# Kernel optimization log

Hardware: AMD Instinct MI355X
Metric: run time of the kernel (lower is better)

## Reference

```python
import jax, jax.numpy as jnp
import numpy as np

NEG_INF = -1e10
LEAKY_ALPHA = 0.2


def setup_inputs() -> dict:
    key = jax.random.key(0)
    k1, k2, k3, k4, k5 = jax.random.split(key, 5)
    N, F, H, D = 4096, 512, 8, 64
    X = jax.random.normal(k1, (N, F), dtype=jnp.float32)
    # dense 0/1 adjacency (float, as used by the mask formula)
    A = jax.random.randint(k2, (N, N), 0, 2).astype(jnp.float32)
    W = jax.random.normal(k3, (H, F, D), dtype=jnp.float32) * (1.0 / np.sqrt(F))
    b = jnp.zeros((H, D), dtype=jnp.float32)
    a_self = jax.random.normal(k4, (H, D), dtype=jnp.float32) * (1.0 / np.sqrt(D))
    a_neigh = jax.random.normal(k5, (H, D), dtype=jnp.float32) * (1.0 / np.sqrt(D))
    return {"X": X, "A": A, "W": W, "b": b, "a_self": a_self, "a_neigh": a_neigh}


def reference(X, A, W, b, a_self, a_neigh):
    # Multi-head dense GAT, heads vectorized. Dropout is identity (eval mode).
    # feats: [H, N, D]
    feats = jnp.einsum('nf,hfd->hnd', X, W)
    e_self = jnp.einsum('hnd,hd->hn', feats, a_self)    # [H, N]
    e_neigh = jnp.einsum('hnd,hd->hn', feats, a_neigh)  # [H, N]
    # outer-sum additive scores: [H, N, N]
    dense = e_self[:, :, None] + e_neigh[:, None, :]
    dense = jnp.where(dense >= 0, dense, LEAKY_ALPHA * dense)  # LeakyReLU(0.2)
    mask = NEG_INF * (1.0 - A)                                  # [N, N]
    dense = dense + mask[None, :, :]
    attn = jax.nn.softmax(dense, axis=-1)                       # [H, N, N]
    out = jnp.einsum('hnm,hmd->hnd', attn, feats) + b[:, None, :]
    # concat heads -> [N, H*D], then relu activation
    H, N, D = out.shape
    out = jnp.transpose(out, (1, 0, 2)).reshape(N, H * D)
    return jax.nn.relu(out)
```

## Files before the change

kernel.cpp:

```cpp
#include <hip/hip_runtime.h>
#include <hip/hip_fp16.h>
#include <stdint.h>


#define NODES 4096
#define FEAT  512
#define HEADS 8
#define DH    64
#define NT    (NODES / 64)

using half2v = __attribute__((ext_vector_type(2))) _Float16;
using half8  = __attribute__((ext_vector_type(8))) _Float16;
using f32x4  = __attribute__((ext_vector_type(4))) float;

__device__ __forceinline__ void gll16(const void* g, void* l) {
    __builtin_amdgcn_global_load_lds(
        (const __attribute__((address_space(1))) uint32_t*)g,
        (__attribute__((address_space(3))) uint32_t*)l, 16, 0, 0);
}

__device__ __forceinline__ uint32_t fenc(float f) {
    uint32_t u = __float_as_uint(f);
    return (u >> 31) ? ~u : (u | 0x80000000u);
}
__device__ __forceinline__ float fdec(uint32_t e) {
    uint32_t u = (e >> 31) ? (e & 0x7FFFFFFFu) : ~e;
    return __uint_as_float(u);
}

#define PACK_BLOCKS 16384
#define CAST_BLOCKS (NODES * FEAT / 4 / 256)
#define WT_BLOCKS   (HEADS * 8)

__global__ __launch_bounds__(256) void prep_kernel(
    const float* __restrict__ A, const float* __restrict__ X, const float* __restrict__ W,
    uint64_t* __restrict__ AbitsT, _Float16* __restrict__ Xh, _Float16* __restrict__ WT,
    uint32_t* __restrict__ enmax_u) {
    __shared__ float t[64][65];
    const int bx = blockIdx.x;
    if (bx < PACK_BLOCKS) {
        const int w    = threadIdx.x >> 6;
        const int lane = threadIdx.x & 63;
        const int v    = bx * 4 + w;
        const int wc   = v >> 10;
        const int rowb = (v & 1023) * 4;
        const float* ar = A + (size_t)wc * 64 + lane;
#pragma unroll
        for (int tt = 0; tt < 4; ++tt) {
            uint64_t m = __ballot(ar[(size_t)(rowb + tt) * NODES] != 0.0f);
            if (lane == 0) AbitsT[(size_t)wc * NODES + rowb + tt] = m;
        }
        return;
    }
    if (bx < PACK_BLOCKS + CAST_BLOCKS) {
        if (bx == PACK_BLOCKS && threadIdx.x < 16) enmax_u[threadIdx.x] = 0;
        int i = ((bx - PACK_BLOCKS) * 256 + threadIdx.x) * 4;
        f32x4 x = *(const f32x4*)(X + i);
        *(half2v*)(Xh + i)     = half2v{(_Float16)x[0], (_Float16)x[1]};
        *(half2v*)(Xh + i + 2) = half2v{(_Float16)x[2], (_Float16)x[3]};
        return;
    }
    const int b2 = bx - PACK_BLOCKS - CAST_BLOCKS;
    const int h  = b2 >> 3;
    const int ft = b2 & 7;
    const int r  = threadIdx.x >> 6;
    const int c  = threadIdx.x & 63;
#pragma unroll
    for (int r0 = 0; r0 < 64; r0 += 4)
        t[r0 + r][c] = W[((size_t)h * FEAT + ft * 64 + r0 + r) * DH + c];
    __syncthreads();
#pragma unroll
    for (int r0 = 0; r0 < 64; r0 += 4)
        WT[((size_t)h * DH + r0 + r) * FEAT + ft * 64 + c] = (_Float16)t[c][r0 + r];
}

__global__ __launch_bounds__(256) void feats_kernel(
    const _Float16* __restrict__ Xh, const _Float16* __restrict__ WT,
    const float* __restrict__ a_self, const float* __restrict__ a_neigh,
    _Float16* __restrict__ Vt, float* __restrict__ e_self,
    _Float16* __restrict__ u_tab, _Float16* __restrict__ v_tab,
    uint32_t* __restrict__ enmax_u) {
    const int h    = blockIdx.y;
    const int bx   = blockIdx.x;
    const int tid  = threadIdx.x;
    const int w    = tid >> 6;
    const int lane = tid & 63;
    const int l15  = lane & 15;
    const int g    = lane >> 4;
    const int n0   = bx * 64 + w * 16;

    f32x4 acc[4] = {};
    const _Float16* xb = Xh + (n0 + l15) * FEAT + g * 8;
    const _Float16* wb = WT + (h * DH + l15) * FEAT + g * 8;

#pragma unroll
    for (int kk = 0; kk < FEAT / 32; ++kk) {
        half8 b = *(const half8*)(xb + kk * 32);
#pragma unroll
        for (int mi = 0; mi < 4; ++mi) {
            half8 a = *(const half8*)(wb + mi * 16 * FEAT + kk * 32);
            acc[mi] = __builtin_amdgcn_mfma_f32_16x16x32_f16(a, b, acc[mi], 0, 0, 0);
        }
    }

    const int cc = w * 2 + (l15 >> 3);
    const int e  = l15 & 7;
    float ps = 0.f, pn = 0.f;
#pragma unroll
    for (int mi = 0; mi < 4; ++mi) {
#pragma unroll
        for (int r = 0; r < 4; ++r) {
            int d = mi * 16 + g * 4 + r;
            float v = acc[mi][r];
            Vt[((size_t)h * NT + bx) * 4096 + cc * 512 + d * 8 + e] = (_Float16)v;
            ps += v * a_self[h * DH + d];
            pn += v * a_neigh[h * DH + d];
        }
    }
    ps += __shfl_xor(ps, 16); ps += __shfl_xor(ps, 32);
    pn += __shfl_xor(pn, 16); pn += __shfl_xor(pn, 32);
    if (g == 0) {
        int n = n0 + l15;
        e_self[h * NODES + n] = ps;
        u_tab[h * NODES + n]  = (_Float16)__expf(pn);
        v_tab[h * NODES + n]  = (_Float16)__expf(0.2f * pn);
    }
    float mx = pn;
    mx = fmaxf(mx, __shfl_xor(mx, 1));
    mx = fmaxf(mx, __shfl_xor(mx, 2));
    mx = fmaxf(mx, __shfl_xor(mx, 4));
    mx = fmaxf(mx, __shfl_xor(mx, 8));
    if (lane == 0) atomicMax(enmax_u + h, fenc(mx));
}

__global__ __launch_bounds__(256, 4) void attn_kernel(
    const uint64_t* __restrict__ AbitsT, const _Float16* __restrict__ Vt,
    const float* __restrict__ e_self, const _Float16* __restrict__ u_tab,
    const _Float16* __restrict__ v_tab, const uint32_t* __restrict__ enmax_u,
    const float* __restrict__ bias, float* __restrict__ out) {
    __shared__ __align__(16) _Float16 Vlds[2][2][4096];
    float* redf = (float*)&Vlds[0][0][0];

    const int tid  = threadIdx.x;
    const int w    = tid >> 6;
    const int lane = tid & 63;
    const int l15  = lane & 15;
    const int g    = lane >> 4;
    const int g8   = g * 8;
    const int rh   = w & 1;
    const int jq   = w >> 1;
    const int h    = blockIdx.x & 7;
    const int i0   = (blockIdx.x >> 3) * 32;

    const float em = fdec(enmax_u[h]);
    const float es = e_self[h * NODES + i0 + rh * 16 + l15];
    const float t0 = es + em;
    const float M  = fmaxf(t0, 0.2f * t0);
    const _Float16 c1 = (_Float16)__expf(es - M);
    const _Float16 c2 = (_Float16)__expf(0.2f * es - M);
    const half2v c1h = half2v{c1, c1};
    const half2v c2h = half2v{c2, c2};

    const _Float16* ub  = u_tab + h * NODES + jq * 2048 + g8;
    const _Float16* vb  = v_tab + h * NODES + jq * 2048 + g8;
    const uint64_t* ab  = AbitsT + (size_t)(jq * 32) * NODES + i0 + rh * 16 + l15;
    const _Float16* vtb = Vt + ((size_t)h * NT + jq * 32) * 4096;

#define STAGE(s_, buf_) do {                                        \
        const _Float16* vs_ = vtb + (size_t)(s_) * 4096;            \
        _Float16* vd_ = &Vlds[jq][buf_][0];                         \
        _Pragma("unroll")                                           \
        for (int p_ = 0; p_ < 4; ++p_) {                            \
            const int c_ = rh * 256 + p_ * 64 + lane;               \
            gll16(vs_ + c_ * 8, vd_ + c_ * 8);                      \
        }                                                           \
    } while (0)

    f32x4 acc[4] = {};
    f32x4 asum = {};
    half8 ones;
#pragma unroll
    for (int e = 0; e < 8; ++e) ones[e] = (_Float16)1.0f;

    STAGE(0, 0);
    uint64_t wb_c = ab[0];
    half8 uf_c[2], vf_c[2];
#pragma unroll
    for (int kk = 0; kk < 2; ++kk) {
        uf_c[kk] = *(const half8*)(ub + kk * 32);
        vf_c[kk] = *(const half8*)(vb + kk * 32);
    }
    __syncthreads();

    for (int s = 0; s < 32; ++s) {
        const int buf = s & 1;
        STAGE(s + 1, buf ^ 1);
        uint64_t wb_n = ab[(size_t)(s + 1) * NODES];
        half8 uf_n[2], vf_n[2];
#pragma unroll
        for (int kk = 0; kk < 2; ++kk) {
            uf_n[kk] = *(const half8*)(ub + (s + 1) * 64 + kk * 32);
            vf_n[kk] = *(const half8*)(vb + (s + 1) * 64 + kk * 32);
        }

        const _Float16* vl = &Vlds[jq][buf][0];
#pragma unroll
        for (int kk = 0; kk < 2; ++kk) {
            const uint32_t b0 = ((uint32_t)(wb_c >> (kk * 32)) >> g8) & 0xFFu;
            half8 paf;
#pragma unroll
            for (int q = 0; q < 4; ++q) {
                half2v u2 = half2v{uf_c[kk][2 * q], uf_c[kk][2 * q + 1]};
                half2v v2 = half2v{vf_c[kk][2 * q], vf_c[kk][2 * q + 1]};
                half2v p2 = __builtin_elementwise_max(u2 * c1h, v2 * c2h);
                uint32_t mlo = (uint32_t)(-(int32_t)((b0 >> (2 * q)) & 1u));
                uint32_t mhi = (uint32_t)(-(int32_t)((b0 >> (2 * q + 1)) & 1u));
                uint32_t m = (mhi & 0xFFFF0000u) | (mlo & 0xFFFFu);
                p2 = __builtin_bit_cast(half2v, __builtin_bit_cast(uint32_t, p2) & m);
                paf[2 * q] = p2[0]; paf[2 * q + 1] = p2[1];
            }
            __builtin_amdgcn_s_setprio(1);
#pragma unroll
            for (int ni = 0; ni < 4; ++ni) {
                const half8 vfr = *(const half8*)(vl + (kk * 4 + g) * 512 + (ni * 16 + l15) * 8);
                acc[ni] = __builtin_amdgcn_mfma_f32_16x16x32_f16(paf, vfr, acc[ni], 0, 0, 0);
            }
            asum = __builtin_amdgcn_mfma_f32_16x16x32_f16(paf, ones, asum, 0, 0, 0);
            __builtin_amdgcn_s_setprio(0);
        }
        wb_c = wb_n;
#pragma unroll
        for (int kk = 0; kk < 2; ++kk) { uf_c[kk] = uf_n[kk]; vf_c[kk] = vf_n[kk]; }
        __syncthreads();
    }

    if (jq == 1) {
#pragma unroll
        for (int ni = 0; ni < 4; ++ni)
#pragma unroll
            for (int r = 0; r < 4; ++r)
                redf[(rh * 16 + g * 4 + r) * 68 + ni * 16 + l15] = acc[ni][r];
        if (l15 == 0) {
#pragma unroll
            for (int r = 0; r < 4; ++r)
                redf[2176 + rh * 16 + g * 4 + r] = asum[r];
        }
    }
    __syncthreads();
    if (jq == 0) {
        float invr[4];
#pragma unroll
        for (int r = 0; r < 4; ++r)
            invr[r] = 1.0f / (asum[r] + redf[2176 + rh * 16 + g * 4 + r]);
#pragma unroll
        for (int ni = 0; ni < 4; ++ni) {
            float bb = bias[h * DH + ni * 16 + l15];
#pragma unroll
            for (int r = 0; r < 4; ++r) {
                float v = (acc[ni][r] + redf[(rh * 16 + g * 4 + r) * 68 + ni * 16 + l15]) * invr[r] + bb;
                out[(size_t)(i0 + rh * 16 + g * 4 + r) * (HEADS * DH) + h * DH + ni * 16 + l15] =
                    fmaxf(v, 0.f);
            }
        }
    }
#undef STAGE
}

extern "C" void kernel_launch(void* const* d_in, const int* in_sizes, int n_in,
                              void* d_out, int out_size, void* d_ws, size_t ws_size,
                              hipStream_t stream) {
    const float* X       = (const float*)d_in[0];
    const float* A       = (const float*)d_in[1];
    const float* W       = (const float*)d_in[2];
    const float* b       = (const float*)d_in[3];
    const float* a_self  = (const float*)d_in[4];
    const float* a_neigh = (const float*)d_in[5];
    float* out = (float*)d_out;

    char* ws = (char*)d_ws;
    size_t off = 0;
    uint64_t* AbitsT = (uint64_t*)(ws + off); off += (size_t)64 * NODES * 8;
    _Float16* Xh     = (_Float16*)(ws + off); off += (size_t)NODES * FEAT * 2;
    _Float16* WT     = (_Float16*)(ws + off); off += (size_t)HEADS * DH * FEAT * 2;
    _Float16* Vt     = (_Float16*)(ws + off); off += (size_t)HEADS * DH * NODES * 2;
    float* e_self    = (float*)(ws + off);    off += (size_t)HEADS * NODES * 4;
    _Float16* u_tab  = (_Float16*)(ws + off); off += (size_t)HEADS * NODES * 2;
    _Float16* v_tab  = (_Float16*)(ws + off); off += (size_t)HEADS * NODES * 2;
    uint32_t* enmax_u = (uint32_t*)(ws + off); off += 64;

    prep_kernel<<<PACK_BLOCKS + CAST_BLOCKS + WT_BLOCKS, 256, 0, stream>>>(
        A, X, W, AbitsT, Xh, WT, enmax_u);
    feats_kernel<<<dim3(NODES / 64, HEADS), 256, 0, stream>>>(
        Xh, WT, a_self, a_neigh, Vt, e_self, u_tab, v_tab, enmax_u);
    attn_kernel<<<(NODES / 32) * HEADS, 256, 0, stream>>>(
        AbitsT, Vt, e_self, u_tab, v_tab, enmax_u, b, out);
}
```

Baseline: 108.9 us.

## Replace bit-packed adjacency with byte-mask layout matched to MFMA fragments

The adjacency is now stored as one byte per entry, laid out in the exact per-lane MFMA fragment order, instead of a transposed 64-bit ballot bitmask. The attention loop loads a 16-byte vector per lane and widens byte masks to half2 masks with v_perm, replacing the per-element shift and negate sequence; it also unrolls the main loop by two. The cost is an 8x larger mask in memory: 16MB written by prep and read by attn for each head, where before it was 2MB. The aim is to cut ALU work inside the inner loop.

```diff
diff --git a/kernel.cpp b/kernel.cpp
--- a/kernel.cpp
+++ b/kernel.cpp
@@ -12,6 +12,13 @@
 using half2v = __attribute__((ext_vector_type(2))) _Float16;
 using half8  = __attribute__((ext_vector_type(8))) _Float16;
 using f32x4  = __attribute__((ext_vector_type(4))) float;
+using u32x4  = __attribute__((ext_vector_type(4))) uint32_t;
+
+#if defined(__has_builtin)
+#if __has_builtin(__builtin_amdgcn_perm)
+#define HAS_PERM 1
+#endif
+#endif
 
 __device__ __forceinline__ void gll16(const void* g, void* l) {
     __builtin_amdgcn_global_load_lds(
@@ -28,32 +35,57 @@
     return __uint_as_float(u);
 }
 
-#define PACK_BLOCKS 16384
+template <int Q>
+__device__ __forceinline__ uint32_t mexpand(uint32_t r) {
+#ifdef HAS_PERM
+    const uint32_t sel = (Q & 1) ? 0x03030202u : 0x01010000u;
+    return __builtin_amdgcn_perm(r, r, sel);
+#else
+    const int sh = (Q & 1) ? 8 : 24;
+    uint32_t lo = (uint32_t)(((int32_t)(r << sh)) >> 31) & 0xFFFFu;
+    uint32_t hi = (uint32_t)(((int32_t)(r << (sh - 8))) >> 31) & 0xFFFF0000u;
+    return lo | hi;
+#endif
+}
+
+#define PACK_BLOCKS 4096
 #define CAST_BLOCKS (NODES * FEAT / 4 / 256)
 #define WT_BLOCKS   (HEADS * 8)
 
 __global__ __launch_bounds__(256) void prep_kernel(
     const float* __restrict__ A, const float* __restrict__ X, const float* __restrict__ W,
-    uint64_t* __restrict__ AbitsT, _Float16* __restrict__ Xh, _Float16* __restrict__ WT,
+    uint8_t* __restrict__ Amask, _Float16* __restrict__ Xh, _Float16* __restrict__ WT,
     uint32_t* __restrict__ enmax_u) {
     __shared__ float t[64][65];
     const int bx = blockIdx.x;
     if (bx < PACK_BLOCKS) {
+        if (bx == 0 && threadIdx.x < 16) enmax_u[threadIdx.x] = 0;
         const int w    = threadIdx.x >> 6;
         const int lane = threadIdx.x & 63;
-        const int v    = bx * 4 + w;
-        const int wc   = v >> 10;
-        const int rowb = (v & 1023) * 4;
-        const float* ar = A + (size_t)wc * 64 + lane;
-#pragma unroll
-        for (int tt = 0; tt < 4; ++tt) {
-            uint64_t m = __ballot(ar[(size_t)(rowb + tt) * NODES] != 0.0f);
-            if (lane == 0) AbitsT[(size_t)wc * NODES + rowb + tt] = m;
-        }
+        const int vidx = bx * 4 + w;
+        const int itile = vidx >> 7;
+        const int wc   = (vidx >> 1) & 63;
+        const int rh   = vidx & 1;
+        const int row  = itile * 32 + rh * 16 + (lane & 15);
+        const int colb = wc * 64 + (lane >> 4) * 8;
+        const float* ap = A + (size_t)row * NODES + colb;
+        f32x4 a0 = *(const f32x4*)(ap);
+        f32x4 a1 = *(const f32x4*)(ap + 4);
+        f32x4 a2 = *(const f32x4*)(ap + 32);
+        f32x4 a3 = *(const f32x4*)(ap + 36);
+        u32x4 o;
+        o[0] = ((a0[0] != 0.f) ? 0xFFu : 0u) | ((a0[1] != 0.f) ? 0xFF00u : 0u) |
+               ((a0[2] != 0.f) ? 0xFF0000u : 0u) | ((a0[3] != 0.f) ? 0xFF000000u : 0u);
+        o[1] = ((a1[0] != 0.f) ? 0xFFu : 0u) | ((a1[1] != 0.f) ? 0xFF00u : 0u) |
+               ((a1[2] != 0.f) ? 0xFF0000u : 0u) | ((a1[3] != 0.f) ? 0xFF000000u : 0u);
+        o[2] = ((a2[0] != 0.f) ? 0xFFu : 0u) | ((a2[1] != 0.f) ? 0xFF00u : 0u) |
+               ((a2[2] != 0.f) ? 0xFF0000u : 0u) | ((a2[3] != 0.f) ? 0xFF000000u : 0u);
+        o[3] = ((a3[0] != 0.f) ? 0xFFu : 0u) | ((a3[1] != 0.f) ? 0xFF00u : 0u) |
+               ((a3[2] != 0.f) ? 0xFF0000u : 0u) | ((a3[3] != 0.f) ? 0xFF000000u : 0u);
+        *(u32x4*)(Amask + ((size_t)vidx * 64 + lane) * 16) = o;
         return;
     }
     if (bx < PACK_BLOCKS + CAST_BLOCKS) {
-        if (bx == PACK_BLOCKS && threadIdx.x < 16) enmax_u[threadIdx.x] = 0;
         int i = ((bx - PACK_BLOCKS) * 256 + threadIdx.x) * 4;
         f32x4 x = *(const f32x4*)(X + i);
         *(half2v*)(Xh + i)     = half2v{(_Float16)x[0], (_Float16)x[1]};
@@ -134,7 +166,7 @@
 }
 
 __global__ __launch_bounds__(256, 4) void attn_kernel(
-    const uint64_t* __restrict__ AbitsT, const _Float16* __restrict__ Vt,
+    const uint8_t* __restrict__ Amask, const _Float16* __restrict__ Vt,
     const float* __restrict__ e_self, const _Float16* __restrict__ u_tab,
     const _Float16* __restrict__ v_tab, const uint32_t* __restrict__ enmax_u,
     const float* __restrict__ bias, float* __restrict__ out) {
@@ -150,7 +182,8 @@
     const int rh   = w & 1;
     const int jq   = w >> 1;
     const int h    = blockIdx.x & 7;
-    const int i0   = (blockIdx.x >> 3) * 32;
+    const int itile = blockIdx.x >> 3;
+    const int i0   = itile * 32;
 
     const float em = fdec(enmax_u[h]);
     const float es = e_self[h * NODES + i0 + rh * 16 + l15];
@@ -163,7 +196,7 @@
 
     const _Float16* ub  = u_tab + h * NODES + jq * 2048 + g8;
     const _Float16* vb  = v_tab + h * NODES + jq * 2048 + g8;
-    const uint64_t* ab  = AbitsT + (size_t)(jq * 32) * NODES + i0 + rh * 16 + l15;
+    const uint8_t* amb = Amask + ((((size_t)itile * 64 + jq * 32) * 2 + rh) * 64 + lane) * 16;
     const _Float16* vtb = Vt + ((size_t)h * NT + jq * 32) * 4096;
 
 #define STAGE(s_, buf_) do {                                        \
@@ -183,7 +216,7 @@
     for (int e = 0; e < 8; ++e) ones[e] = (_Float16)1.0f;
 
     STAGE(0, 0);
-    uint64_t wb_c = ab[0];
+    u32x4 mk_c = *(const u32x4*)(amb);
     half8 uf_c[2], vf_c[2];
 #pragma unroll
     for (int kk = 0; kk < 2; ++kk) {
@@ -192,10 +225,11 @@
     }
     __syncthreads();
 
+#pragma unroll 2
     for (int s = 0; s < 32; ++s) {
         const int buf = s & 1;
         STAGE(s + 1, buf ^ 1);
-        uint64_t wb_n = ab[(size_t)(s + 1) * NODES];
+        u32x4 mk_n = *(const u32x4*)(amb + (size_t)(s + 1) * 2048);
         half8 uf_n[2], vf_n[2];
 #pragma unroll
         for (int kk = 0; kk < 2; ++kk) {
@@ -206,16 +240,14 @@
         const _Float16* vl = &Vlds[jq][buf][0];
 #pragma unroll
         for (int kk = 0; kk < 2; ++kk) {
-            const uint32_t b0 = ((uint32_t)(wb_c >> (kk * 32)) >> g8) & 0xFFu;
             half8 paf;
 #pragma unroll
             for (int q = 0; q < 4; ++q) {
                 half2v u2 = half2v{uf_c[kk][2 * q], uf_c[kk][2 * q + 1]};
                 half2v v2 = half2v{vf_c[kk][2 * q], vf_c[kk][2 * q + 1]};
                 half2v p2 = __builtin_elementwise_max(u2 * c1h, v2 * c2h);
-                uint32_t mlo = (uint32_t)(-(int32_t)((b0 >> (2 * q)) & 1u));
-                uint32_t mhi = (uint32_t)(-(int32_t)((b0 >> (2 * q + 1)) & 1u));
-                uint32_t m = (mhi & 0xFFFF0000u) | (mlo & 0xFFFFu);
+                const uint32_t r = mk_c[kk * 2 + (q >> 1)];
+                const uint32_t m = (q & 1) ? mexpand<1>(r) : mexpand<0>(r);
                 p2 = __builtin_bit_cast(half2v, __builtin_bit_cast(uint32_t, p2) & m);
                 paf[2 * q] = p2[0]; paf[2 * q + 1] = p2[1];
             }
@@ -228,7 +260,7 @@
             asum = __builtin_amdgcn_mfma_f32_16x16x32_f16(paf, ones, asum, 0, 0, 0);
             __builtin_amdgcn_s_setprio(0);
         }
-        wb_c = wb_n;
+        mk_c = mk_n;
 #pragma unroll
         for (int kk = 0; kk < 2; ++kk) { uf_c[kk] = uf_n[kk]; vf_c[kk] = vf_n[kk]; }
         __syncthreads();
@@ -279,19 +311,19 @@
 
     char* ws = (char*)d_ws;
     size_t off = 0;
-    uint64_t* AbitsT = (uint64_t*)(ws + off); off += (size_t)64 * NODES * 8;
+    uint8_t* Amask   = (uint8_t*)(ws + off);  off += (size_t)NODES * NODES + 8192;
     _Float16* Xh     = (_Float16*)(ws + off); off += (size_t)NODES * FEAT * 2;
     _Float16* WT     = (_Float16*)(ws + off); off += (size_t)HEADS * DH * FEAT * 2;
     _Float16* Vt     = (_Float16*)(ws + off); off += (size_t)HEADS * DH * NODES * 2;
     float* e_self    = (float*)(ws + off);    off += (size_t)HEADS * NODES * 4;
     _Float16* u_tab  = (_Float16*)(ws + off); off += (size_t)HEADS * NODES * 2;
     _Float16* v_tab  = (_Float16*)(ws + off); off += (size_t)HEADS * NODES * 2;
-    uint32_t* enmax_u = (uint32_t*)(ws + off); off += 64;
+    uint32_t* enmax_u = (uint32_t*)(ws + off); off += 8192;
 
     prep_kernel<<<PACK_BLOCKS + CAST_BLOCKS + WT_BLOCKS, 256, 0, stream>>>(
-        A, X, W, AbitsT, Xh, WT, enmax_u);
+        A, X, W, Amask, Xh, WT, enmax_u);
     feats_kernel<<<dim3(NODES / 64, HEADS), 256, 0, stream>>>(
         Xh, WT, a_self, a_neigh, Vt, e_self, u_tab, v_tab, enmax_u);
     attn_kernel<<<(NODES / 32) * HEADS, 256, 0, stream>>>(
-        AbitsT, Vt, e_self, u_tab, v_tab, enmax_u, b, out);
-}
+        Amask, Vt, e_self, u_tab, v_tab, enmax_u, b, out);
+}
```

New measurement: 99.01 us. 9.1% less time.
